# Optimization experiments

Measured on AMD Instinct MI355X. Metric: run time of the kernel, lower is better.

Reference implementation:

```python
import jax, jax.numpy as jnp
import numpy as np

D_X = 1024
D_TEXT = 768
FUSION_DIM = D_X + D_TEXT  # 1792
M = 16
K = 2


def setup_inputs() -> dict:
    key = jax.random.key(0)
    k1, k2, k3, k4, k5 = jax.random.split(key, 5)
    B, H, W = 256, 32, 32
    x = jax.random.normal(k1, (B, D_X, H, W), dtype=jnp.float32)
    degraded = jax.random.normal(k2, (B, D_TEXT), dtype=jnp.float32)
    # learned params (random so routing is non-trivial)
    w_fusion = jax.random.normal(k3, (FUSION_DIM, FUSION_DIM), dtype=jnp.float32) * (1.0 / np.sqrt(FUSION_DIM))
    b_fusion = jax.random.normal(k4, (FUSION_DIM,), dtype=jnp.float32) * 0.01
    w_gate = jax.random.normal(k5, (FUSION_DIM, M), dtype=jnp.float32) * 0.02
    return {"x": x, "degraded": degraded, "w_fusion": w_fusion,
            "b_fusion": b_fusion, "w_gate": w_gate}


def reference(x, degraded, w_fusion, b_fusion, w_gate):
    B = x.shape[0]
    # global average pool over H,W -> [B, d_x]
    x_pooled = jnp.mean(x, axis=(2, 3))
    fused = jnp.concatenate([x_pooled, degraded], axis=1)        # [B, d_x+d_text]
    fused = jnp.dot(fused, w_fusion) + b_fusion                  # Linear
    fused = jax.nn.gelu(fused, approximate=False)                # exact GELU (torch default)
    clean_logits = jnp.dot(fused, w_gate)                        # [B, M]
    probs_for_mi = jax.nn.softmax(clean_logits, axis=1)
    # eval path: logits = clean_logits (no noise)
    num_consider = min(K + 1, M)
    top_logits, top_indices = jax.lax.top_k(clean_logits, num_consider)
    top_k_logits = top_logits[:, :K]
    top_k_indices = top_indices[:, :K]
    top_k_gates = jax.nn.softmax(top_k_logits, axis=1)
    rows = jnp.arange(B)[:, None]
    gates = jnp.zeros_like(clean_logits).at[rows, top_k_indices].set(top_k_gates)
    moe_loss = jnp.float32(0.0)
    return gates, moe_loss, probs_for_mi, top_k_indices
```

## Files before the change

kernel.cpp:

```cpp
#include <hip/hip_runtime.h>
#include <math.h>

#define D_X      1024
#define D_TEXT   768
#define FDIM     1792
#define BATCH    256
#define M_EXP    16
#define HW_TOT   1024

#define OUT_GATES 0
#define OUT_LOSS  4096
#define OUT_PROBS 4097
#define OUT_IDX   8193

__global__ __launch_bounds__(256) void pool_kernel(const float* __restrict__ x,
                                                   float* __restrict__ fused) {
    const int gtid = blockIdx.x * 256 + threadIdx.x;
    const int wave = gtid >> 6;
    const int lane = gtid & 63;
    const float4* xr = reinterpret_cast<const float4*>(x + (size_t)wave * HW_TOT);
    float s = 0.0f;
#pragma unroll
    for (int k = 0; k < 4; ++k) {
        float4 v = xr[k * 64 + lane];
        s += v.x + v.y + v.z + v.w;
    }
#pragma unroll
    for (int off = 32; off > 0; off >>= 1) s += __shfl_xor(s, off, 64);
    if (lane == 0) {
        const int b = wave >> 10;
        const int c = wave & 1023;
        fused[(size_t)b * FDIM + c] = s * (1.0f / 1024.0f);
    }
}

__global__ __launch_bounds__(256) void copy_deg_kernel(const float* __restrict__ deg,
                                                       float* __restrict__ fused) {
    const int tid = blockIdx.x * 256 + threadIdx.x;
    if (tid >= BATCH * (D_TEXT / 4)) return;
    const int b  = tid / (D_TEXT / 4);
    const int j4 = tid % (D_TEXT / 4);
    const float4 v = reinterpret_cast<const float4*>(deg)[tid];
    reinterpret_cast<float4*>(fused)[(size_t)b * (FDIM / 4) + (D_X / 4) + j4] = v;
}

#define BM 32
#define BN 64
#define BK 32

__global__ __launch_bounds__(256) void gemm_gelu_kernel(const float* __restrict__ A,
                                                        const float* __restrict__ W,
                                                        const float* __restrict__ bias,
                                                        float* __restrict__ C) {
    __shared__ float As[BK][BM];
    __shared__ float Ws[BK][BN];

    const int tid = threadIdx.x;
    const int tx = tid & 15;
    const int ty = tid >> 4;
    const int m0 = blockIdx.x * BM;
    const int n0 = blockIdx.y * BN;

    float acc[2][4] = {};

    for (int k0 = 0; k0 < FDIM; k0 += BK) {
        {
            const int row = tid >> 3;
            const int kk4 = (tid & 7) * 4;
            float4 v = *reinterpret_cast<const float4*>(A + (size_t)(m0 + row) * FDIM + k0 + kk4);
            As[kk4 + 0][row] = v.x;
            As[kk4 + 1][row] = v.y;
            As[kk4 + 2][row] = v.z;
            As[kk4 + 3][row] = v.w;
        }
#pragma unroll
        for (int i = 0; i < 2; ++i) {
            const int id = i * 256 + tid;
            const int kk = id >> 4;
            const int n4 = (id & 15) * 4;
            *reinterpret_cast<float4*>(&Ws[kk][n4]) =
                *reinterpret_cast<const float4*>(W + (size_t)(k0 + kk) * FDIM + n0 + n4);
        }
        __syncthreads();

#pragma unroll
        for (int kk = 0; kk < BK; ++kk) {
            const float2 a = *reinterpret_cast<const float2*>(&As[kk][ty * 2]);
            const float4 w = *reinterpret_cast<const float4*>(&Ws[kk][tx * 4]);
            const float av[2] = {a.x, a.y};
            const float wv[4] = {w.x, w.y, w.z, w.w};
#pragma unroll
            for (int i = 0; i < 2; ++i)
#pragma unroll
                for (int j = 0; j < 4; ++j)
                    acc[i][j] = fmaf(av[i], wv[j], acc[i][j]);
        }
        __syncthreads();
    }

#pragma unroll
    for (int i = 0; i < 2; ++i) {
        const int m = m0 + ty * 2 + i;
#pragma unroll
        for (int j = 0; j < 4; ++j) {
            const int n = n0 + tx * 4 + j;
            const float v = acc[i][j] + bias[n];
            const float g = v * 0.5f * (1.0f + erff(v * 0.70710678118654752440f));
            C[(size_t)m * FDIM + n] = g;
        }
    }
}

__global__ __launch_bounds__(256) void gate_kernel(const float* __restrict__ act,
                                                   const float* __restrict__ wg,
                                                   float* __restrict__ out) {
    const int b = blockIdx.x;
    const int tid = threadIdx.x;

    float p[M_EXP];
#pragma unroll
    for (int m = 0; m < M_EXP; ++m) p[m] = 0.0f;

    for (int k = tid; k < FDIM; k += 256) {
        const float a = act[(size_t)b * FDIM + k];
        const float4* wr = reinterpret_cast<const float4*>(wg + (size_t)k * M_EXP);
#pragma unroll
        for (int q = 0; q < 4; ++q) {
            const float4 w = wr[q];
            p[q * 4 + 0] = fmaf(a, w.x, p[q * 4 + 0]);
            p[q * 4 + 1] = fmaf(a, w.y, p[q * 4 + 1]);
            p[q * 4 + 2] = fmaf(a, w.z, p[q * 4 + 2]);
            p[q * 4 + 3] = fmaf(a, w.w, p[q * 4 + 3]);
        }
    }

#pragma unroll
    for (int off = 32; off > 0; off >>= 1) {
#pragma unroll
        for (int m = 0; m < M_EXP; ++m) p[m] += __shfl_xor(p[m], off, 64);
    }

    __shared__ float red[4][M_EXP];
    const int wid = tid >> 6;
    const int lane = tid & 63;
    if (lane == 0) {
#pragma unroll
        for (int m = 0; m < M_EXP; ++m) red[wid][m] = p[m];
    }
    __syncthreads();

    if (tid == 0) {
        float l[M_EXP];
#pragma unroll
        for (int m = 0; m < M_EXP; ++m)
            l[m] = red[0][m] + red[1][m] + red[2][m] + red[3][m];

        float mx = l[0];
#pragma unroll
        for (int m = 1; m < M_EXP; ++m) mx = fmaxf(mx, l[m]);
        float e[M_EXP], s = 0.0f;
#pragma unroll
        for (int m = 0; m < M_EXP; ++m) { e[m] = expf(l[m] - mx); s += e[m]; }
        const float inv = 1.0f / s;
#pragma unroll
        for (int m = 0; m < M_EXP; ++m) out[OUT_PROBS + b * M_EXP + m] = e[m] * inv;

        int i0 = 0; float v0 = l[0];
#pragma unroll
        for (int m = 1; m < M_EXP; ++m) if (l[m] > v0) { v0 = l[m]; i0 = m; }
        int i1 = -1; float v1 = -INFINITY;
#pragma unroll
        for (int m = 0; m < M_EXP; ++m) if (m != i0 && l[m] > v1) { v1 = l[m]; i1 = m; }

        const float t = expf(v1 - v0);
        const float g0 = 1.0f / (1.0f + t);
        const float g1 = t * g0;

#pragma unroll
        for (int m = 0; m < M_EXP; ++m) out[OUT_GATES + b * M_EXP + m] = 0.0f;
        out[OUT_GATES + b * M_EXP + i0] = g0;
        out[OUT_GATES + b * M_EXP + i1] = g1;

        out[OUT_IDX + b * 2 + 0] = (float)i0;
        out[OUT_IDX + b * 2 + 1] = (float)i1;

        if (b == 0) out[OUT_LOSS] = 0.0f;
    }
}

extern "C" void kernel_launch(void* const* d_in, const int* in_sizes, int n_in,
                              void* d_out, int out_size, void* d_ws, size_t ws_size,
                              hipStream_t stream) {
    const float* x        = (const float*)d_in[0];
    const float* degraded = (const float*)d_in[1];
    const float* w_fusion = (const float*)d_in[2];
    const float* b_fusion = (const float*)d_in[3];
    const float* w_gate   = (const float*)d_in[4];
    float* out = (float*)d_out;

    float* fused = (float*)d_ws;
    float* actb  = fused + (size_t)BATCH * FDIM;

    pool_kernel<<<(BATCH * D_X) / 4, 256, 0, stream>>>(x, fused);

    copy_deg_kernel<<<192, 256, 0, stream>>>(degraded, fused);

    gemm_gelu_kernel<<<dim3(BATCH / BM, FDIM / BN), 256, 0, stream>>>(fused, w_fusion, b_fusion, actb);

    gate_kernel<<<BATCH, 256, 0, stream>>>(actb, w_gate, out);
}
```

Before: 264.8 us.

## Fuse gate projection into GEMM epilogue, double-buffer GEMM, merge pool/copy kernels

The pooling and text-copy kernels are merged into one launch. The GEMM now uses BK=64 with register-prefetched double-buffered shared memory. Its epilogue computes GELU into shared memory and multiplies by the matching slice of w_gate, writing per-column-block partial logits. A small finalize kernel sums those partials and does the softmax and top-2, which removes the separate activation round-trip and gate kernel. This adds a partial-sum buffer and more shared memory per block, which can lower occupancy.

```diff
diff --git a/kernel.cpp b/kernel.cpp
--- a/kernel.cpp
+++ b/kernel.cpp
@@ -13,47 +13,78 @@
 #define OUT_PROBS 4097
 #define OUT_IDX   8193
 
-__global__ __launch_bounds__(256) void pool_kernel(const float* __restrict__ x,
-                                                   float* __restrict__ fused) {
-    const int gtid = blockIdx.x * 256 + threadIdx.x;
-    const int wave = gtid >> 6;
-    const int lane = gtid & 63;
-    const float4* xr = reinterpret_cast<const float4*>(x + (size_t)wave * HW_TOT);
-    float s = 0.0f;
-#pragma unroll
-    for (int k = 0; k < 4; ++k) {
-        float4 v = xr[k * 64 + lane];
-        s += v.x + v.y + v.z + v.w;
-    }
-#pragma unroll
-    for (int off = 32; off > 0; off >>= 1) s += __shfl_xor(s, off, 64);
-    if (lane == 0) {
-        const int b = wave >> 10;
-        const int c = wave & 1023;
-        fused[(size_t)b * FDIM + c] = s * (1.0f / 1024.0f);
-    }
-}
-
-__global__ __launch_bounds__(256) void copy_deg_kernel(const float* __restrict__ deg,
-                                                       float* __restrict__ fused) {
-    const int tid = blockIdx.x * 256 + threadIdx.x;
-    if (tid >= BATCH * (D_TEXT / 4)) return;
-    const int b  = tid / (D_TEXT / 4);
-    const int j4 = tid % (D_TEXT / 4);
-    const float4 v = reinterpret_cast<const float4*>(deg)[tid];
-    reinterpret_cast<float4*>(fused)[(size_t)b * (FDIM / 4) + (D_X / 4) + j4] = v;
+#define NBLK_POOL (BATCH * D_X / 4)
+#define NBLK_COPY 192
+
+__global__ __launch_bounds__(256) void pool_copy_kernel(const float* __restrict__ x,
+                                                        const float* __restrict__ deg,
+                                                        float* __restrict__ fused) {
+    const int blk = blockIdx.x;
+    if (blk < NBLK_POOL) {
+        const int gtid = blk * 256 + threadIdx.x;
+        const int row  = gtid >> 6;
+        const int lane = gtid & 63;
+        const float4* xr = reinterpret_cast<const float4*>(x + (size_t)row * HW_TOT);
+        float s = 0.0f;
+#pragma unroll
+        for (int k = 0; k < 4; ++k) {
+            float4 v = xr[k * 64 + lane];
+            s += v.x + v.y + v.z + v.w;
+        }
+#pragma unroll
+        for (int off = 32; off > 0; off >>= 1) s += __shfl_xor(s, off, 64);
+        if (lane == 0) {
+            const int b = row >> 10;
+            const int c = row & 1023;
+            fused[(size_t)b * FDIM + c] = s * (1.0f / 1024.0f);
+        }
+    } else {
+        const int tid = (blk - NBLK_POOL) * 256 + threadIdx.x;
+        if (tid < BATCH * (D_TEXT / 4)) {
+            const int b  = tid / (D_TEXT / 4);
+            const int j4 = tid % (D_TEXT / 4);
+            const float4 v = reinterpret_cast<const float4*>(deg)[tid];
+            reinterpret_cast<float4*>(fused)[(size_t)b * (FDIM / 4) + (D_X / 4) + j4] = v;
+        }
+    }
 }
 
 #define BM 32
 #define BN 64
-#define BK 32
-
-__global__ __launch_bounds__(256) void gemm_gelu_kernel(const float* __restrict__ A,
+#define BK 64
+#define NITER (FDIM / BK)
+
+#define LOADA(k0)                                                                     \
+    pa0 = *reinterpret_cast<const float4*>(A + (size_t)(m0 + ar) * FDIM + (k0) + ak4);       \
+    pa1 = *reinterpret_cast<const float4*>(A + (size_t)(m0 + ar + 16) * FDIM + (k0) + ak4);
+
+#define LOADW(k0)                                                                     \
+    pw0 = *reinterpret_cast<const float4*>(W + (size_t)((k0) + wr0) * FDIM + n0 + wc4);      \
+    pw1 = *reinterpret_cast<const float4*>(W + (size_t)((k0) + wr0 + 16) * FDIM + n0 + wc4); \
+    pw2 = *reinterpret_cast<const float4*>(W + (size_t)((k0) + wr0 + 32) * FDIM + n0 + wc4); \
+    pw3 = *reinterpret_cast<const float4*>(W + (size_t)((k0) + wr0 + 48) * FDIM + n0 + wc4);
+
+#define STOREA(buf)                                                                   \
+    As[buf][ak4 + 0][ar] = pa0.x; As[buf][ak4 + 1][ar] = pa0.y;                       \
+    As[buf][ak4 + 2][ar] = pa0.z; As[buf][ak4 + 3][ar] = pa0.w;                       \
+    As[buf][ak4 + 0][ar + 16] = pa1.x; As[buf][ak4 + 1][ar + 16] = pa1.y;             \
+    As[buf][ak4 + 2][ar + 16] = pa1.z; As[buf][ak4 + 3][ar + 16] = pa1.w;
+
+#define STOREW(buf)                                                                   \
+    *reinterpret_cast<float4*>(&Ws[buf][wr0][wc4])      = pw0;                        \
+    *reinterpret_cast<float4*>(&Ws[buf][wr0 + 16][wc4]) = pw1;                        \
+    *reinterpret_cast<float4*>(&Ws[buf][wr0 + 32][wc4]) = pw2;                        \
+    *reinterpret_cast<float4*>(&Ws[buf][wr0 + 48][wc4]) = pw3;
+
+__global__ __launch_bounds__(256) void gemm_gate_kernel(const float* __restrict__ A,
                                                         const float* __restrict__ W,
                                                         const float* __restrict__ bias,
-                                                        float* __restrict__ C) {
-    __shared__ float As[BK][BM];
-    __shared__ float Ws[BK][BN];
+                                                        const float* __restrict__ wg,
+                                                        float* __restrict__ part) {
+    __shared__ float As[2][BK][BM + 1];
+    __shared__ float Ws[2][BK][BN];
+    __shared__ float wgs[BN][M_EXP];
+    __shared__ float actS[BM][BN + 1];
 
     const int tid = threadIdx.x;
     const int tx = tid & 15;
@@ -61,131 +92,130 @@
     const int m0 = blockIdx.x * BM;
     const int n0 = blockIdx.y * BN;
 
+    {
+        const int r  = tid >> 2;
+        const int c4 = (tid & 3) * 4;
+        *reinterpret_cast<float4*>(&wgs[r][c4]) =
+            *reinterpret_cast<const float4*>(wg + (size_t)(n0 + r) * M_EXP + c4);
+    }
+
+    const int ar  = tid >> 4;
+    const int ak4 = (tid & 15) * 4;
+    const int wr0 = tid >> 4;
+    const int wc4 = (tid & 15) * 4;
+
+    float4 pa0, pa1, pw0, pw1, pw2, pw3;
+
+    LOADA(0); LOADW(0);
+    STOREA(0); STOREW(0);
+    LOADA(BK); LOADW(BK);
+    __syncthreads();
+
     float acc[2][4] = {};
-
-    for (int k0 = 0; k0 < FDIM; k0 += BK) {
-        {
-            const int row = tid >> 3;
-            const int kk4 = (tid & 7) * 4;
-            float4 v = *reinterpret_cast<const float4*>(A + (size_t)(m0 + row) * FDIM + k0 + kk4);
-            As[kk4 + 0][row] = v.x;
-            As[kk4 + 1][row] = v.y;
-            As[kk4 + 2][row] = v.z;
-            As[kk4 + 3][row] = v.w;
-        }
-#pragma unroll
-        for (int i = 0; i < 2; ++i) {
-            const int id = i * 256 + tid;
-            const int kk = id >> 4;
-            const int n4 = (id & 15) * 4;
-            *reinterpret_cast<float4*>(&Ws[kk][n4]) =
-                *reinterpret_cast<const float4*>(W + (size_t)(k0 + kk) * FDIM + n0 + n4);
-        }
-        __syncthreads();
-
+    int cur = 0;
+
+    for (int t = 0; t < NITER; ++t) {
 #pragma unroll
         for (int kk = 0; kk < BK; ++kk) {
-            const float2 a = *reinterpret_cast<const float2*>(&As[kk][ty * 2]);
-            const float4 w = *reinterpret_cast<const float4*>(&Ws[kk][tx * 4]);
-            const float av[2] = {a.x, a.y};
-            const float wv[4] = {w.x, w.y, w.z, w.w};
-#pragma unroll
-            for (int i = 0; i < 2; ++i)
-#pragma unroll
-                for (int j = 0; j < 4; ++j)
-                    acc[i][j] = fmaf(av[i], wv[j], acc[i][j]);
-        }
-        __syncthreads();
+            const float2 a = *reinterpret_cast<const float2*>(&As[cur][kk][ty * 2]);
+            const float4 w = *reinterpret_cast<const float4*>(&Ws[cur][kk][tx * 4]);
+            acc[0][0] = fmaf(a.x, w.x, acc[0][0]);
+            acc[0][1] = fmaf(a.x, w.y, acc[0][1]);
+            acc[0][2] = fmaf(a.x, w.z, acc[0][2]);
+            acc[0][3] = fmaf(a.x, w.w, acc[0][3]);
+            acc[1][0] = fmaf(a.y, w.x, acc[1][0]);
+            acc[1][1] = fmaf(a.y, w.y, acc[1][1]);
+            acc[1][2] = fmaf(a.y, w.z, acc[1][2]);
+            acc[1][3] = fmaf(a.y, w.w, acc[1][3]);
+        }
+        if (t < NITER - 1) {
+            const int nxt = cur ^ 1;
+            STOREA(nxt); STOREW(nxt);
+            if (t < NITER - 2) {
+                const int k0 = (t + 2) * BK;
+                LOADA(k0); LOADW(k0);
+            }
+            __syncthreads();
+            cur = nxt;
+        }
     }
 
 #pragma unroll
     for (int i = 0; i < 2; ++i) {
-        const int m = m0 + ty * 2 + i;
+        const int m = ty * 2 + i;
 #pragma unroll
         for (int j = 0; j < 4; ++j) {
-            const int n = n0 + tx * 4 + j;
-            const float v = acc[i][j] + bias[n];
-            const float g = v * 0.5f * (1.0f + erff(v * 0.70710678118654752440f));
-            C[(size_t)m * FDIM + n] = g;
-        }
-    }
-}
-
-__global__ __launch_bounds__(256) void gate_kernel(const float* __restrict__ act,
-                                                   const float* __restrict__ wg,
-                                                   float* __restrict__ out) {
-    const int b = blockIdx.x;
-    const int tid = threadIdx.x;
-
-    float p[M_EXP];
-#pragma unroll
-    for (int m = 0; m < M_EXP; ++m) p[m] = 0.0f;
-
-    for (int k = tid; k < FDIM; k += 256) {
-        const float a = act[(size_t)b * FDIM + k];
-        const float4* wr = reinterpret_cast<const float4*>(wg + (size_t)k * M_EXP);
+            const int n = tx * 4 + j;
+            const float v = acc[i][j] + bias[n0 + n];
+            actS[m][n] = v * 0.5f * (1.0f + erff(v * 0.70710678118654752440f));
+        }
+    }
+    __syncthreads();
+
+    const int pm = tid >> 3;
+    const int pe = (tid & 7) * 2;
+    float s0 = 0.0f, s1 = 0.0f;
+#pragma unroll
+    for (int n = 0; n < BN; ++n) {
+        const float a = actS[pm][n];
+        s0 = fmaf(a, wgs[n][pe], s0);
+        s1 = fmaf(a, wgs[n][pe + 1], s1);
+    }
+    float* pr = part + ((size_t)blockIdx.y * BATCH + (m0 + pm)) * M_EXP + pe;
+    pr[0] = s0;
+    pr[1] = s1;
+}
+
+__global__ __launch_bounds__(64) void finalize_kernel(const float* __restrict__ part,
+                                                      float* __restrict__ out) {
+    const int b = blockIdx.x * 64 + threadIdx.x;
+
+    float l[M_EXP];
+#pragma unroll
+    for (int m = 0; m < M_EXP; ++m) l[m] = 0.0f;
+
+    for (int nb = 0; nb < NITER; ++nb) {
+        const float4* pr = reinterpret_cast<const float4*>(part + ((size_t)nb * BATCH + b) * M_EXP);
 #pragma unroll
         for (int q = 0; q < 4; ++q) {
-            const float4 w = wr[q];
-            p[q * 4 + 0] = fmaf(a, w.x, p[q * 4 + 0]);
-            p[q * 4 + 1] = fmaf(a, w.y, p[q * 4 + 1]);
-            p[q * 4 + 2] = fmaf(a, w.z, p[q * 4 + 2]);
-            p[q * 4 + 3] = fmaf(a, w.w, p[q * 4 + 3]);
-        }
-    }
-
-#pragma unroll
-    for (int off = 32; off > 0; off >>= 1) {
-#pragma unroll
-        for (int m = 0; m < M_EXP; ++m) p[m] += __shfl_xor(p[m], off, 64);
-    }
-
-    __shared__ float red[4][M_EXP];
-    const int wid = tid >> 6;
-    const int lane = tid & 63;
-    if (lane == 0) {
-#pragma unroll
-        for (int m = 0; m < M_EXP; ++m) red[wid][m] = p[m];
-    }
-    __syncthreads();
-
-    if (tid == 0) {
-        float l[M_EXP];
-#pragma unroll
-        for (int m = 0; m < M_EXP; ++m)
-            l[m] = red[0][m] + red[1][m] + red[2][m] + red[3][m];
-
-        float mx = l[0];
-#pragma unroll
-        for (int m = 1; m < M_EXP; ++m) mx = fmaxf(mx, l[m]);
-        float e[M_EXP], s = 0.0f;
-#pragma unroll
-        for (int m = 0; m < M_EXP; ++m) { e[m] = expf(l[m] - mx); s += e[m]; }
-        const float inv = 1.0f / s;
-#pragma unroll
-        for (int m = 0; m < M_EXP; ++m) out[OUT_PROBS + b * M_EXP + m] = e[m] * inv;
-
-        int i0 = 0; float v0 = l[0];
-#pragma unroll
-        for (int m = 1; m < M_EXP; ++m) if (l[m] > v0) { v0 = l[m]; i0 = m; }
-        int i1 = -1; float v1 = -INFINITY;
-#pragma unroll
-        for (int m = 0; m < M_EXP; ++m) if (m != i0 && l[m] > v1) { v1 = l[m]; i1 = m; }
-
-        const float t = expf(v1 - v0);
-        const float g0 = 1.0f / (1.0f + t);
-        const float g1 = t * g0;
-
-#pragma unroll
-        for (int m = 0; m < M_EXP; ++m) out[OUT_GATES + b * M_EXP + m] = 0.0f;
-        out[OUT_GATES + b * M_EXP + i0] = g0;
-        out[OUT_GATES + b * M_EXP + i1] = g1;
-
-        out[OUT_IDX + b * 2 + 0] = (float)i0;
-        out[OUT_IDX + b * 2 + 1] = (float)i1;
-
-        if (b == 0) out[OUT_LOSS] = 0.0f;
-    }
+            const float4 v = pr[q];
+            l[q * 4 + 0] += v.x;
+            l[q * 4 + 1] += v.y;
+            l[q * 4 + 2] += v.z;
+            l[q * 4 + 3] += v.w;
+        }
+    }
+
+    float mx = l[0];
+#pragma unroll
+    for (int m = 1; m < M_EXP; ++m) mx = fmaxf(mx, l[m]);
+    float e[M_EXP], s = 0.0f;
+#pragma unroll
+    for (int m = 0; m < M_EXP; ++m) { e[m] = expf(l[m] - mx); s += e[m]; }
+    const float inv = 1.0f / s;
+#pragma unroll
+    for (int m = 0; m < M_EXP; ++m) out[OUT_PROBS + b * M_EXP + m] = e[m] * inv;
+
+    int i0 = 0; float v0 = l[0];
+#pragma unroll
+    for (int m = 1; m < M_EXP; ++m) if (l[m] > v0) { v0 = l[m]; i0 = m; }
+    int i1 = -1; float v1 = -INFINITY;
+#pragma unroll
+    for (int m = 0; m < M_EXP; ++m) if (m != i0 && l[m] > v1) { v1 = l[m]; i1 = m; }
+
+    const float t = expf(v1 - v0);
+    const float g0 = 1.0f / (1.0f + t);
+    const float g1 = t * g0;
+
+#pragma unroll
+    for (int m = 0; m < M_EXP; ++m) out[OUT_GATES + b * M_EXP + m] = 0.0f;
+    out[OUT_GATES + b * M_EXP + i0] = g0;
+    out[OUT_GATES + b * M_EXP + i1] = g1;
+
+    out[OUT_IDX + b * 2 + 0] = (float)i0;
+    out[OUT_IDX + b * 2 + 1] = (float)i1;
+
+    if (b == 0) out[OUT_LOSS] = 0.0f;
 }
 
 extern "C" void kernel_launch(void* const* d_in, const int* in_sizes, int n_in,
@@ -199,13 +229,11 @@
     float* out = (float*)d_out;
 
     float* fused = (float*)d_ws;
-    float* actb  = fused + (size_t)BATCH * FDIM;
-
-    pool_kernel<<<(BATCH * D_X) / 4, 256, 0, stream>>>(x, fused);
-
-    copy_deg_kernel<<<192, 256, 0, stream>>>(degraded, fused);
-
-    gemm_gelu_kernel<<<dim3(BATCH / BM, FDIM / BN), 256, 0, stream>>>(fused, w_fusion, b_fusion, actb);
-
-    gate_kernel<<<BATCH, 256, 0, stream>>>(actb, w_gate, out);
-}
+    float* part  = fused + (size_t)BATCH * FDIM;
+
+    pool_copy_kernel<<<NBLK_POOL + NBLK_COPY, 256, 0, stream>>>(x, degraded, fused);
+
+    gemm_gate_kernel<<<dim3(BATCH / BM, FDIM / BN), 256, 0, stream>>>(fused, w_fusion, b_fusion, w_gate, part);
+
+    finalize_kernel<<<BATCH / 64, 64, 0, stream>>>(part, out);
+}
```

Measured after the change: 250.1 us. 5.6% less time.
